# Performance work log

Hardware: AMD Instinct MI355X
Metric: run time of the kernel (lower is better)

Reference implementation:

```python
import jax, jax.numpy as jnp
import numpy as np


def _conv1x1(x, W, b):
    # x: [B,C,H,W], W: [O,C], b: [O]  -> [B,O,H,W]
    return jnp.einsum('bchw,oc->bohw', x, W) + b[None, :, None, None]


def setup_inputs() -> dict:
    key = jax.random.key(0)
    ks = jax.random.split(key, 8)
    B, C, H, W = 16, 512, 48, 48
    d = C // 8
    scale = 0.02
    return {
        'feat_map': jax.random.normal(ks[0], (B, C, H, W), dtype=jnp.float32),
        'Wq': jax.random.normal(ks[1], (d, C), dtype=jnp.float32) * scale,
        'bq': jax.random.normal(ks[2], (d,), dtype=jnp.float32) * scale,
        'Wk': jax.random.normal(ks[3], (d, C), dtype=jnp.float32) * scale,
        'bk': jax.random.normal(ks[4], (d,), dtype=jnp.float32) * scale,
        'Wv': jax.random.normal(ks[5], (C, C), dtype=jnp.float32) * scale,
        'bv': jax.random.normal(ks[6], (C,), dtype=jnp.float32) * scale,
        'gamma': jnp.ones((1,), dtype=jnp.float32),
    }


def reference(feat_map, Wq, bq, Wk, bk, Wv, bv, gamma):
    # SAModule (DANet spatial attention):
    #   q = conv1(x) -> [B, d, HW] -> permute [B, HW, d]
    #   k = conv2(x) -> [B, d, HW]
    #   attn = softmax(q @ k, axis=-1)            # [B, HW, HW]
    #   v = conv3(x) -> [B, C, HW]
    #   out = v @ attn^T -> [B, C, H, W]
    #   y = gamma * out + x
    B, C, H, W = feat_map.shape
    HW = H * W
    q = _conv1x1(feat_map, Wq, bq).reshape(B, -1, HW).transpose(0, 2, 1)  # [B,HW,d]
    k = _conv1x1(feat_map, Wk, bk).reshape(B, -1, HW)                     # [B,d,HW]
    attn = jax.nn.softmax(jnp.einsum('bnd,bdm->bnm', q, k), axis=-1)      # [B,HW,HW]
    v = _conv1x1(feat_map, Wv, bv).reshape(B, C, HW)                      # [B,C,HW]
    out = jnp.einsum('bcm,bnm->bcn', v, attn).reshape(B, C, H, W)
    return gamma * out + feat_map
```

## Files before the change

kernel.cpp:

```cpp
#include <hip/hip_runtime.h>

typedef __bf16 bf16x8 __attribute__((ext_vector_type(8)));
typedef __bf16 bf16x4 __attribute__((ext_vector_type(4)));
typedef float  f32x4  __attribute__((ext_vector_type(4)));

constexpr int kHW = 2304;
constexpr int kC  = 512;

#if __has_builtin(__builtin_amdgcn_exp2f)
#define EXP2(x) __builtin_amdgcn_exp2f(x)
#else
#define EXP2(x) exp2f(x)
#endif

__device__ __forceinline__ void dma16(const __bf16* g, __bf16* l) {
    __builtin_amdgcn_global_load_lds(
        (const volatile __attribute__((address_space(1))) void*)g,
        (volatile __attribute__((address_space(3))) void*)l, 16, 0, 0);
}

__global__ void pack_weights(const float* __restrict__ Wq, const float* __restrict__ Wk,
                             const float* __restrict__ Wv, __bf16* __restrict__ Wqk2,
                             __bf16* __restrict__ Wvb2) {
    int idx = blockIdx.x * 256 + threadIdx.x;
    int o = idx >> 9, k = idx & 511, kb = k >> 6, kr = k & 63;
    if (idx < 64 * 512) {
        Wqk2[((size_t)kb * 128 + o) * 72 + kr]      = (__bf16)Wq[idx];
        Wqk2[((size_t)kb * 128 + 64 + o) * 72 + kr] = (__bf16)Wk[idx];
    }
    if (idx < 512 * 512)
        Wvb2[((size_t)kb * 512 + o) * 72 + kr] = (__bf16)Wv[idx];
}

__global__ void pack_x(const float* __restrict__ x, __bf16* __restrict__ XT2) {
    __shared__ __bf16 tile[64][65];
    int n0 = blockIdx.x * 64, kblk = blockIdx.y, b = blockIdx.z;
    int c0 = kblk * 64;
    int t = threadIdx.x;
    const float* xb = x + (size_t)b * kC * kHW;
#pragma unroll
    for (int rep = 0; rep < 16; ++rep) {
        int c_loc = rep * 4 + (t >> 6);
        int n_loc = t & 63;
        tile[c_loc][n_loc] = (__bf16)xb[(size_t)(c0 + c_loc) * kHW + n0 + n_loc];
    }
    __syncthreads();
    __bf16* dst = XT2 + ((size_t)b * 8 + kblk) * kHW * 72;
#pragma unroll
    for (int rep = 0; rep < 2; ++rep) {
        int item = rep * 256 + t;
        int n_loc = item >> 3, chunk = item & 7;
        bf16x8 v;
#pragma unroll
        for (int j = 0; j < 8; ++j) v[j] = tile[chunk * 8 + j][n_loc];
        *(bf16x8*)(dst + (size_t)(n0 + n_loc) * 72 + chunk * 8) = v;
    }
}

__global__ __launch_bounds__(256) void qkv_gemm(const __bf16* __restrict__ XT2,
                                                const __bf16* __restrict__ Wqk2,
                                                const __bf16* __restrict__ Wvb2,
                                                const float* __restrict__ bq,
                                                const float* __restrict__ bk,
                                                const float* __restrict__ bv,
                                                __bf16* __restrict__ qbuf,
                                                __bf16* __restrict__ kbuf,
                                                __bf16* __restrict__ vbuf2) {
    __shared__ __align__(16) __bf16 A_lds[128 * 72];
    __shared__ __align__(16) __bf16 B_lds[128 * 72];
    int r0 = blockIdx.x * 128, type = blockIdx.y, b = blockIdx.z;
    int t = threadIdx.x, wave = t >> 6, lane = t & 63, quad = lane >> 4, l16 = lane & 15;

    f32x4 acc[8][2];
#pragma unroll
    for (int i = 0; i < 8; ++i)
#pragma unroll
        for (int j = 0; j < 2; ++j) acc[i][j] = (f32x4){0.f, 0.f, 0.f, 0.f};

    for (int kb = 0; kb < 8; ++kb) {
        const __bf16* Asrc;
        const __bf16* Bsrc;
        if (type == 0) {
            Asrc = XT2 + (((size_t)b * 8 + kb) * kHW + r0) * 72;
            Bsrc = Wqk2 + (size_t)kb * 128 * 72;
        } else {
            Asrc = Wvb2 + ((size_t)kb * 512 + (type - 1) * 128) * 72;
            Bsrc = XT2 + (((size_t)b * 8 + kb) * kHW + r0) * 72;
        }
        __syncthreads();
        for (int ch = wave; ch < 18; ch += 4) {
            dma16(Asrc + ch * 512 + lane * 8, &A_lds[ch * 512]);
            dma16(Bsrc + ch * 512 + lane * 8, &B_lds[ch * 512]);
        }
        __syncthreads();
#pragma unroll
        for (int dk = 0; dk < 2; ++dk) {
            bf16x8 bfr[2];
#pragma unroll
            for (int ct = 0; ct < 2; ++ct)
                bfr[ct] = *(const bf16x8*)(&B_lds[(wave * 32 + ct * 16 + l16) * 72 + dk * 32 + quad * 8]);
#pragma unroll
            for (int rt = 0; rt < 8; ++rt) {
                bf16x8 a = *(const bf16x8*)(&A_lds[(rt * 16 + l16) * 72 + dk * 32 + quad * 8]);
#pragma unroll
                for (int ct = 0; ct < 2; ++ct)
                    acc[rt][ct] = __builtin_amdgcn_mfma_f32_16x16x32_bf16(a, bfr[ct], acc[rt][ct], 0, 0, 0);
            }
        }
    }

    if (type == 0) {
        constexpr float kLog2e = 1.4426950408889634f;
#pragma unroll
        for (int ct = 0; ct < 2; ++ct) {
            int o = wave * 32 + ct * 16 + l16;
            float bias = (o < 64) ? bq[o] : bk[o - 64];
            float scale = (o < 64) ? kLog2e : 1.0f;
#pragma unroll
            for (int rt = 0; rt < 8; ++rt)
#pragma unroll
                for (int r = 0; r < 4; ++r) {
                    int n = r0 + rt * 16 + quad * 4 + r;
                    __bf16 val = (__bf16)((acc[rt][ct][r] + bias) * scale);
                    if (o < 64)
                        qbuf[((size_t)b * kHW + n) * 64 + o] = val;
                    else
                        kbuf[(((size_t)b * 36 + (n >> 6)) * 64 + (n & 63)) * 72 + (o - 64)] = val;
                }
        }
    } else {
#pragma unroll
        for (int rt = 0; rt < 8; ++rt)
#pragma unroll
            for (int r = 0; r < 4; ++r) {
                int c = (type - 1) * 128 + rt * 16 + quad * 4 + r;
                float bias = bv[c];
#pragma unroll
                for (int ct = 0; ct < 2; ++ct) {
                    int m = r0 + wave * 32 + ct * 16 + l16;
                    vbuf2[(((size_t)b * 36 + (m >> 6)) * 512 + c) * 72 + (m & 63)] = (__bf16)(acc[rt][ct][r] + bias);
                }
            }
    }
}

__global__ __launch_bounds__(256, 2) void attn_kernel(const __bf16* __restrict__ qbuf,
                                                      const __bf16* __restrict__ kbuf,
                                                      const __bf16* __restrict__ vbuf2,
                                                      const float* __restrict__ x,
                                                      const float* __restrict__ gamma,
                                                      float* __restrict__ out) {
    __shared__ __align__(16) __bf16 K_lds[2][64 * 72];
    __shared__ __align__(16) __bf16 V_lds[2][128 * 72];
    __shared__ __align__(16) __bf16 P_lds[128 * 72];
    __shared__ float rs_lds[128];

    int n0 = blockIdx.x * 128, c0 = blockIdx.y * 128, b = blockIdx.z;
    int t = threadIdx.x, wave = t >> 6, lane = t & 63, quad = lane >> 4, l16 = lane & 15;
    const __bf16* q_b    = qbuf + (size_t)b * kHW * 64;
    const __bf16* k_base = kbuf + (size_t)b * 36 * 64 * 72;

    bf16x8 aq[2][2];
#pragma unroll
    for (int rt2 = 0; rt2 < 2; ++rt2)
#pragma unroll
        for (int dk = 0; dk < 2; ++dk)
            aq[rt2][dk] = *(const bf16x8*)(q_b + (size_t)(n0 + wave * 32 + rt2 * 16 + l16) * 64 + dk * 32 + quad * 8);

    f32x4 acc[2][8];
#pragma unroll
    for (int i = 0; i < 2; ++i)
#pragma unroll
        for (int j = 0; j < 8; ++j) acc[i][j] = (f32x4){0.f, 0.f, 0.f, 0.f};
    float rsum[2] = {0.f, 0.f};

    auto issue_dma = [&](int i, int buf) {
        const __bf16* ks = k_base + (size_t)i * 64 * 72;
        const __bf16* vs = vbuf2 + (((size_t)b * 36 + i) * 512 + c0) * 72;
        for (int ch = wave; ch < 9; ch += 4)
            dma16(ks + ch * 512 + lane * 8, &K_lds[buf][ch * 512]);
        for (int ch = wave; ch < 18; ch += 4)
            dma16(vs + ch * 512 + lane * 8, &V_lds[buf][ch * 512]);
    };

    issue_dma(0, 0);
    for (int i = 0; i < 36; ++i) {
        int buf = i & 1;
        __syncthreads();
        if (i + 1 < 36) issue_dma(i + 1, buf ^ 1);

        __bf16* prow = &P_lds[(wave * 32 + l16) * 72 + quad * 4];
#pragma unroll
        for (int mt = 0; mt < 4; ++mt) {
            bf16x8 kf0 = *(const bf16x8*)(&K_lds[buf][(mt * 16 + l16) * 72 + quad * 8]);
            bf16x8 kf1 = *(const bf16x8*)(&K_lds[buf][(mt * 16 + l16) * 72 + 32 + quad * 8]);
#pragma unroll
            for (int rt2 = 0; rt2 < 2; ++rt2) {
                f32x4 s = (f32x4){0.f, 0.f, 0.f, 0.f};
                s = __builtin_amdgcn_mfma_f32_16x16x32_bf16(kf0, aq[rt2][0], s, 0, 0, 0);
                s = __builtin_amdgcn_mfma_f32_16x16x32_bf16(kf1, aq[rt2][1], s, 0, 0, 0);
                bf16x4 pv;
                float part = 0.f;
#pragma unroll
                for (int r = 0; r < 4; ++r) {
                    pv[r] = (__bf16)EXP2(s[r]);
                    part += (float)pv[r];
                }
                rsum[rt2] += part;
                *(bf16x4*)(prow + rt2 * 16 * 72 + mt * 16) = pv;
            }
        }

        bf16x8 pf[2][2];
#pragma unroll
        for (int rt2 = 0; rt2 < 2; ++rt2)
#pragma unroll
            for (int dk = 0; dk < 2; ++dk)
                pf[rt2][dk] = *(const bf16x8*)(&P_lds[(wave * 32 + rt2 * 16 + l16) * 72 + dk * 32 + quad * 8]);
        __builtin_amdgcn_s_setprio(1);
#pragma unroll
        for (int ct = 0; ct < 8; ++ct) {
            bf16x8 vf0 = *(const bf16x8*)(&V_lds[buf][(ct * 16 + l16) * 72 + quad * 8]);
            bf16x8 vf1 = *(const bf16x8*)(&V_lds[buf][(ct * 16 + l16) * 72 + 32 + quad * 8]);
            acc[0][ct] = __builtin_amdgcn_mfma_f32_16x16x32_bf16(pf[0][0], vf0, acc[0][ct], 0, 0, 0);
            acc[0][ct] = __builtin_amdgcn_mfma_f32_16x16x32_bf16(pf[0][1], vf1, acc[0][ct], 0, 0, 0);
            acc[1][ct] = __builtin_amdgcn_mfma_f32_16x16x32_bf16(pf[1][0], vf0, acc[1][ct], 0, 0, 0);
            acc[1][ct] = __builtin_amdgcn_mfma_f32_16x16x32_bf16(pf[1][1], vf1, acc[1][ct], 0, 0, 0);
        }
        __builtin_amdgcn_s_setprio(0);
    }

#pragma unroll
    for (int rt2 = 0; rt2 < 2; ++rt2) {
        float v = rsum[rt2];
        v += __shfl_xor(v, 16);
        v += __shfl_xor(v, 32);
        if (quad == 0) rs_lds[wave * 32 + rt2 * 16 + l16] = v;
    }
    __syncthreads();

    float g = gamma[0];
    const float* x_b = x + (size_t)b * kC * kHW;
    float* out_b = out + (size_t)b * kC * kHW;
#pragma unroll
    for (int rt2 = 0; rt2 < 2; ++rt2) {
        float inv[4];
#pragma unroll
        for (int r = 0; r < 4; ++r) inv[r] = 1.f / rs_lds[wave * 32 + rt2 * 16 + quad * 4 + r];
#pragma unroll
        for (int ct = 0; ct < 8; ++ct) {
            int c = c0 + ct * 16 + l16;
            size_t base = (size_t)c * kHW + n0 + wave * 32 + rt2 * 16 + quad * 4;
            f32x4 xin = *(const f32x4*)(x_b + base);
            f32x4 y;
#pragma unroll
            for (int r = 0; r < 4; ++r) y[r] = g * acc[rt2][ct][r] * inv[r] + xin[r];
            *(f32x4*)(out_b + base) = y;
        }
    }
}

extern "C" void kernel_launch(void* const* d_in, const int* in_sizes, int n_in,
                              void* d_out, int out_size, void* d_ws, size_t ws_size,
                              hipStream_t stream) {
    const float* x     = (const float*)d_in[0];
    const float* Wq    = (const float*)d_in[1];
    const float* bq    = (const float*)d_in[2];
    const float* Wk    = (const float*)d_in[3];
    const float* bk    = (const float*)d_in[4];
    const float* Wv    = (const float*)d_in[5];
    const float* bv    = (const float*)d_in[6];
    const float* gamma = (const float*)d_in[7];
    float* out = (float*)d_out;

    char* ws = (char*)d_ws;
    __bf16* XT2   = (__bf16*)(ws);
    __bf16* Wqk2  = (__bf16*)(ws + 42467328);
    __bf16* Wvb2  = (__bf16*)(ws + 42614784);
    __bf16* qbuf  = (__bf16*)(ws + 43204608);
    __bf16* kbuf  = (__bf16*)(ws + 47923200);
    __bf16* vbuf2 = (__bf16*)(ws + 53231616);

    hipLaunchKernelGGL(pack_weights, dim3(1024), dim3(256), 0, stream, Wq, Wk, Wv, Wqk2, Wvb2);
    hipLaunchKernelGGL(pack_x, dim3(36, 8, 16), dim3(256), 0, stream, x, XT2);
    hipLaunchKernelGGL(qkv_gemm, dim3(18, 5, 16), dim3(256), 0, stream,
                       XT2, Wqk2, Wvb2, bq, bk, bv, qbuf, kbuf, vbuf2);
    hipLaunchKernelGGL(attn_kernel, dim3(18, 4, 16), dim3(256), 0, stream,
                       qbuf, kbuf, vbuf2, x, gamma, out);
}
```

Measured before the change: 410.2 us.

## Halve attention key tile to 32 with XOR-swizzled K layout for higher occupancy

Shrinks the per-iteration key tile in the attention kernel from 64 to 32 positions. K is stored unpadded with an XOR swizzle to avoid LDS bank conflicts, and V and P use a 40-element padded stride; the qkv_gemm output layouts change to match. LDS use drops to roughly half, so launch bounds rise to 4 blocks per CU for more occupancy and latency hiding. The cost is twice as many loop iterations and barriers, plus less MFMA work per synchronization.

```diff
diff --git a/kernel.cpp b/kernel.cpp
--- a/kernel.cpp
+++ b/kernel.cpp
@@ -122,10 +122,13 @@
                 for (int r = 0; r < 4; ++r) {
                     int n = r0 + rt * 16 + quad * 4 + r;
                     __bf16 val = (__bf16)((acc[rt][ct][r] + bias) * scale);
-                    if (o < 64)
+                    if (o < 64) {
                         qbuf[((size_t)b * kHW + n) * 64 + o] = val;
-                    else
-                        kbuf[(((size_t)b * 36 + (n >> 6)) * 64 + (n & 63)) * 72 + (o - 64)] = val;
+                    } else {
+                        int d = o - 64;
+                        int dsw = (((d >> 3) ^ (n & 7)) << 3) | (d & 7);
+                        kbuf[(((size_t)b * 72 + (n >> 5)) * 32 + (n & 31)) * 64 + dsw] = val;
+                    }
                 }
         }
     } else {
@@ -138,27 +141,27 @@
 #pragma unroll
                 for (int ct = 0; ct < 2; ++ct) {
                     int m = r0 + wave * 32 + ct * 16 + l16;
-                    vbuf2[(((size_t)b * 36 + (m >> 6)) * 512 + c) * 72 + (m & 63)] = (__bf16)(acc[rt][ct][r] + bias);
+                    vbuf2[(((size_t)b * 72 + (m >> 5)) * 512 + c) * 40 + (m & 31)] = (__bf16)(acc[rt][ct][r] + bias);
                 }
             }
     }
 }
 
-__global__ __launch_bounds__(256, 2) void attn_kernel(const __bf16* __restrict__ qbuf,
+__global__ __launch_bounds__(256, 4) void attn_kernel(const __bf16* __restrict__ qbuf,
                                                       const __bf16* __restrict__ kbuf,
                                                       const __bf16* __restrict__ vbuf2,
                                                       const float* __restrict__ x,
                                                       const float* __restrict__ gamma,
                                                       float* __restrict__ out) {
-    __shared__ __align__(16) __bf16 K_lds[2][64 * 72];
-    __shared__ __align__(16) __bf16 V_lds[2][128 * 72];
-    __shared__ __align__(16) __bf16 P_lds[128 * 72];
+    __shared__ __align__(16) __bf16 K_lds[2][32 * 64];
+    __shared__ __align__(16) __bf16 V_lds[2][128 * 40];
+    __shared__ __align__(16) __bf16 P_lds[128 * 40];
     __shared__ float rs_lds[128];
 
     int n0 = blockIdx.x * 128, c0 = blockIdx.y * 128, b = blockIdx.z;
     int t = threadIdx.x, wave = t >> 6, lane = t & 63, quad = lane >> 4, l16 = lane & 15;
     const __bf16* q_b    = qbuf + (size_t)b * kHW * 64;
-    const __bf16* k_base = kbuf + (size_t)b * 36 * 64 * 72;
+    const __bf16* k_base = kbuf + (size_t)b * 72 * 32 * 64;
 
     bf16x8 aq[2][2];
 #pragma unroll
@@ -175,25 +178,26 @@
     float rsum[2] = {0.f, 0.f};
 
     auto issue_dma = [&](int i, int buf) {
-        const __bf16* ks = k_base + (size_t)i * 64 * 72;
-        const __bf16* vs = vbuf2 + (((size_t)b * 36 + i) * 512 + c0) * 72;
-        for (int ch = wave; ch < 9; ch += 4)
-            dma16(ks + ch * 512 + lane * 8, &K_lds[buf][ch * 512]);
-        for (int ch = wave; ch < 18; ch += 4)
+        const __bf16* ks = k_base + (size_t)i * 32 * 64;
+        const __bf16* vs = vbuf2 + (((size_t)b * 72 + i) * 512 + c0) * 40;
+        dma16(ks + wave * 512 + lane * 8, &K_lds[buf][wave * 512]);
+        for (int ch = wave; ch < 10; ch += 4)
             dma16(vs + ch * 512 + lane * 8, &V_lds[buf][ch * 512]);
     };
 
     issue_dma(0, 0);
-    for (int i = 0; i < 36; ++i) {
+    for (int i = 0; i < 72; ++i) {
         int buf = i & 1;
         __syncthreads();
-        if (i + 1 < 36) issue_dma(i + 1, buf ^ 1);
-
-        __bf16* prow = &P_lds[(wave * 32 + l16) * 72 + quad * 4];
-#pragma unroll
-        for (int mt = 0; mt < 4; ++mt) {
-            bf16x8 kf0 = *(const bf16x8*)(&K_lds[buf][(mt * 16 + l16) * 72 + quad * 8]);
-            bf16x8 kf1 = *(const bf16x8*)(&K_lds[buf][(mt * 16 + l16) * 72 + 32 + quad * 8]);
+        if (i + 1 < 72) issue_dma(i + 1, buf ^ 1);
+
+        __bf16* prow = &P_lds[(wave * 32 + l16) * 40 + quad * 4];
+#pragma unroll
+        for (int mt = 0; mt < 2; ++mt) {
+            int row = mt * 16 + l16;
+            int sw = (row & 7) << 3;
+            bf16x8 kf0 = *(const bf16x8*)(&K_lds[buf][row * 64 + ((quad * 8) ^ sw)]);
+            bf16x8 kf1 = *(const bf16x8*)(&K_lds[buf][row * 64 + ((32 + quad * 8) ^ sw)]);
 #pragma unroll
             for (int rt2 = 0; rt2 < 2; ++rt2) {
                 f32x4 s = (f32x4){0.f, 0.f, 0.f, 0.f};
@@ -207,25 +211,20 @@
                     part += (float)pv[r];
                 }
                 rsum[rt2] += part;
-                *(bf16x4*)(prow + rt2 * 16 * 72 + mt * 16) = pv;
+                *(bf16x4*)(prow + rt2 * 16 * 40 + mt * 16) = pv;
             }
         }
 
-        bf16x8 pf[2][2];
+        bf16x8 pf[2];
 #pragma unroll
         for (int rt2 = 0; rt2 < 2; ++rt2)
-#pragma unroll
-            for (int dk = 0; dk < 2; ++dk)
-                pf[rt2][dk] = *(const bf16x8*)(&P_lds[(wave * 32 + rt2 * 16 + l16) * 72 + dk * 32 + quad * 8]);
+            pf[rt2] = *(const bf16x8*)(&P_lds[(wave * 32 + rt2 * 16 + l16) * 40 + quad * 8]);
         __builtin_amdgcn_s_setprio(1);
 #pragma unroll
         for (int ct = 0; ct < 8; ++ct) {
-            bf16x8 vf0 = *(const bf16x8*)(&V_lds[buf][(ct * 16 + l16) * 72 + quad * 8]);
-            bf16x8 vf1 = *(const bf16x8*)(&V_lds[buf][(ct * 16 + l16) * 72 + 32 + quad * 8]);
-            acc[0][ct] = __builtin_amdgcn_mfma_f32_16x16x32_bf16(pf[0][0], vf0, acc[0][ct], 0, 0, 0);
-            acc[0][ct] = __builtin_amdgcn_mfma_f32_16x16x32_bf16(pf[0][1], vf1, acc[0][ct], 0, 0, 0);
-            acc[1][ct] = __builtin_amdgcn_mfma_f32_16x16x32_bf16(pf[1][0], vf0, acc[1][ct], 0, 0, 0);
-            acc[1][ct] = __builtin_amdgcn_mfma_f32_16x16x32_bf16(pf[1][1], vf1, acc[1][ct], 0, 0, 0);
+            bf16x8 vf = *(const bf16x8*)(&V_lds[buf][(ct * 16 + l16) * 40 + quad * 8]);
+            acc[0][ct] = __builtin_amdgcn_mfma_f32_16x16x32_bf16(pf[0], vf, acc[0][ct], 0, 0, 0);
+            acc[1][ct] = __builtin_amdgcn_mfma_f32_16x16x32_bf16(pf[1], vf, acc[1][ct], 0, 0, 0);
         }
         __builtin_amdgcn_s_setprio(0);
     }
@@ -279,7 +278,7 @@
     __bf16* Wvb2  = (__bf16*)(ws + 42614784);
     __bf16* qbuf  = (__bf16*)(ws + 43204608);
     __bf16* kbuf  = (__bf16*)(ws + 47923200);
-    __bf16* vbuf2 = (__bf16*)(ws + 53231616);
+    __bf16* vbuf2 = (__bf16*)(ws + 52641792);
 
     hipLaunchKernelGGL(pack_weights, dim3(1024), dim3(256), 0, stream, Wq, Wk, Wv, Wqk2, Wvb2);
     hipLaunchKernelGGL(pack_x, dim3(36, 8, 16), dim3(256), 0, stream, x, XT2);
```

Result: faster. 400.6 us (-2.3%).
